# Optimization experiments

Measured on AMD Instinct MI355X. Metric: run time of the kernel, lower is better.

Reference implementation:

```python
import jax, jax.numpy as jnp
import numpy as np

D_MODEL = 1024
N_HEADS = 16
D_HEAD = D_MODEL // N_HEADS
D_FF = 4096
B, T = 2, 2048
EPS = 1e-6


def setup_inputs() -> dict:
    key = jax.random.key(0)
    ks = jax.random.split(key, 10)
    s = 0.02
    return {
        "x": jax.random.normal(ks[0], (B, T, D_MODEL), dtype=jnp.float32),
        # Linear weights stored as (in, out) so y = x @ W (equivalent to torch x @ W.T)
        "Wq": jax.random.normal(ks[1], (D_MODEL, D_MODEL), dtype=jnp.float32) * s,
        "Wk": jax.random.normal(ks[2], (D_MODEL, D_MODEL), dtype=jnp.float32) * s,
        "Wv": jax.random.normal(ks[3], (D_MODEL, D_MODEL), dtype=jnp.float32) * s,
        "Wo": jax.random.normal(ks[4], (D_MODEL, D_MODEL), dtype=jnp.float32) * s,
        "W1": jax.random.normal(ks[5], (D_MODEL, D_FF), dtype=jnp.float32) * s,
        "b1": jnp.zeros((D_FF,), dtype=jnp.float32),
        "W2": jax.random.normal(ks[6], (D_FF, D_MODEL), dtype=jnp.float32) * s,
        "b2": jnp.zeros((D_MODEL,), dtype=jnp.float32),
        "g1": jnp.ones((D_MODEL,), dtype=jnp.float32),
        "g2": jnp.ones((D_MODEL,), dtype=jnp.float32),
    }


def rmsnorm(x, g):
    return x * jax.lax.rsqrt(jnp.mean(x * x, axis=-1, keepdims=True) + EPS) * g


def attention(x, Wq, Wk, Wv, Wo):
    b, t, c = x.shape
    def split_heads(y):  # [B,T,C] -> [B,H,T,Dh]
        return y.reshape(b, t, N_HEADS, D_HEAD).transpose(0, 2, 1, 3)
    q = split_heads(x @ Wq)
    k = split_heads(x @ Wk)
    v = split_heads(x @ Wv)
    att = jnp.einsum("bhqd,bhkd->bhqk", q, k) / jnp.sqrt(jnp.float32(D_HEAD))
    causal = jnp.tril(jnp.ones((t, t), dtype=bool))
    att = jnp.where(causal[None, None], att, -jnp.inf)
    att = jax.nn.softmax(att, axis=-1)
    y = jnp.einsum("bhqk,bhkd->bhqd", att, v)
    y = y.transpose(0, 2, 1, 3).reshape(b, t, c)
    return y @ Wo


def reference(x, Wq, Wk, Wv, Wo, W1, b1, W2, b2, g1, g2):
    x = x + attention(rmsnorm(x, g1), Wq, Wk, Wv, Wo)
    h = rmsnorm(x, g2)
    h = jax.nn.gelu(h @ W1 + b1, approximate=False) @ W2 + b2
    return x + h
```

## Files before the change

### kernel.cpp

```cpp
#include <hip/hip_runtime.h>
#include <hip/hip_bf16.h>
#include <math.h>
#include <stdint.h>


typedef __bf16 v8bf  __attribute__((ext_vector_type(8)));
typedef float  v4f   __attribute__((ext_vector_type(4)));

#define T_SEQ 2048
#define EXP2F(x) __builtin_amdgcn_exp2f(x)

#define FRAG(base, R, ko) \
  (*(const v8bf*)((base) + (R) * 64 + (((((ko) >> 3) ^ ((R) & 7))) << 3)))

__device__ __forceinline__ void async_ld16(const void* g, void* l) {
  __builtin_amdgcn_global_load_lds(
      (const __attribute__((address_space(1))) uint32_t*)g,
      (__attribute__((address_space(3))) uint32_t*)l, 16, 0, 0);
}

__global__ __launch_bounds__(256) void transpose_w(
    const float* __restrict__ W, __hip_bfloat16* __restrict__ WT,
    int K, int N, int ldo)
{
  __shared__ float tile[32][33];
  const int n0 = blockIdx.x * 32, k0 = blockIdx.y * 32;
  const int tx = threadIdx.x, ty = threadIdx.y;
#pragma unroll
  for (int i = 0; i < 32; i += 8)
    tile[ty + i][tx] = W[(size_t)(k0 + ty + i) * N + n0 + tx];
  __syncthreads();
#pragma unroll
  for (int i = 0; i < 32; i += 8)
    WT[(size_t)(n0 + ty + i) * ldo + k0 + tx] = __float2bfloat16(tile[tx][ty + i]);
}

__global__ __launch_bounds__(256) void transpose_v(
    const __hip_bfloat16* __restrict__ QKV, __hip_bfloat16* __restrict__ VTg)
{
  __shared__ float tile[32][33];
  const int t0 = blockIdx.x * 32;
  const int bh = blockIdx.y >> 1;
  const int dt = (blockIdx.y & 1) * 32;
  const int b = bh >> 4, h = bh & 15;
  const int tx = threadIdx.x, ty = threadIdx.y;
#pragma unroll
  for (int i = 0; i < 32; i += 8)
    tile[ty + i][tx] = __bfloat162float(
        QKV[(size_t)(b * T_SEQ + t0 + ty + i) * 3072 + 2048 + h * 64 + dt + tx]);
  __syncthreads();
#pragma unroll
  for (int i = 0; i < 32; i += 8)
    VTg[((size_t)bh * 64 + dt + ty + i) * T_SEQ + t0 + tx] =
        __float2bfloat16(tile[tx][ty + i]);
}

__global__ __launch_bounds__(256) void rmsnorm_kernel(
    const float* __restrict__ x, const float* __restrict__ g,
    __hip_bfloat16* __restrict__ out)
{
  const int row = blockIdx.x;
  const int t = threadIdx.x;
  const float4 v = ((const float4*)(x + (size_t)row * 1024))[t];
  float ss = v.x * v.x + v.y * v.y + v.z * v.z + v.w * v.w;
#pragma unroll
  for (int off = 32; off; off >>= 1) ss += __shfl_xor(ss, off, 64);
  __shared__ float red[4];
  if ((t & 63) == 0) red[t >> 6] = ss;
  __syncthreads();
  ss = red[0] + red[1] + red[2] + red[3];
  const float rs = rsqrtf(ss * (1.0f / 1024.0f) + 1e-6f);
  const float4 gv = ((const float4*)g)[t];
  __hip_bfloat16* o = out + (size_t)row * 1024 + t * 4;
  o[0] = __float2bfloat16(v.x * rs * gv.x);
  o[1] = __float2bfloat16(v.y * rs * gv.y);
  o[2] = __float2bfloat16(v.z * rs * gv.z);
  o[3] = __float2bfloat16(v.w * rs * gv.w);
}

template <int MODE, int MT>
__global__ __launch_bounds__(256, 2) void gemm_bt(
    const __hip_bfloat16* __restrict__ A,
    const __hip_bfloat16* __restrict__ BT,
    const float* __restrict__ bias,
    const float* __restrict__ resid,
    __hip_bfloat16* __restrict__ outb,
    float* __restrict__ outf,
    int M, int N, int K)
{
  __shared__ __align__(16) __hip_bfloat16 As[32 * MT * 64];
  __shared__ __align__(16) __hip_bfloat16 Bs[128 * 64];
  const int tid = threadIdx.x;
  const int wave = tid >> 6, lane = tid & 63;
  const int quad = lane >> 4, l16 = lane & 15;
  const int m0 = blockIdx.y * (32 * MT), n0 = blockIdx.x * 128;
  const int wr = (wave >> 1) * (16 * MT), wc = (wave & 1) * 64;
  const int lrow = lane >> 3;
  const int scol = ((lane & 7) ^ lrow) * 8;

  v4f acc[MT][4];
#pragma unroll
  for (int i = 0; i < MT; i++)
#pragma unroll
    for (int j = 0; j < 4; j++)
#pragma unroll
      for (int c = 0; c < 4; c++) acc[i][j][c] = 0.0f;

  for (int k0 = 0; k0 < K; k0 += 64) {
#pragma unroll
    for (int i = 0; i < MT + 4; i++) {
      const int c = wave * (MT + 4) + i;
      if (c < 4 * MT) {
        async_ld16(A + (size_t)(m0 + c * 8 + lrow) * K + k0 + scol, As + c * 512);
      } else {
        const int cb = c - 4 * MT;
        async_ld16(BT + (size_t)(n0 + cb * 8 + lrow) * K + k0 + scol, Bs + cb * 512);
      }
    }
    __syncthreads();
#pragma unroll
    for (int ks = 0; ks < 64; ks += 32) {
      v8bf af[MT], bf[4];
#pragma unroll
      for (int mt = 0; mt < MT; mt++)
        af[mt] = FRAG(As, wr + mt * 16 + l16, ks + quad * 8);
#pragma unroll
      for (int nt = 0; nt < 4; nt++)
        bf[nt] = FRAG(Bs, wc + nt * 16 + l16, ks + quad * 8);
#pragma unroll
      for (int mt = 0; mt < MT; mt++)
#pragma unroll
        for (int nt = 0; nt < 4; nt++)
          acc[mt][nt] = __builtin_amdgcn_mfma_f32_16x16x32_bf16(
              af[mt], bf[nt], acc[mt][nt], 0, 0, 0);
    }
    __syncthreads();
  }

#pragma unroll
  for (int mt = 0; mt < MT; mt++) {
#pragma unroll
    for (int r = 0; r < 4; r++) {
      const int gm = m0 + wr + mt * 16 + quad * 4 + r;
#pragma unroll
      for (int nt = 0; nt < 4; nt++) {
        const int gn = n0 + wc + nt * 16 + l16;
        float v = acc[mt][nt][r];
        if (MODE == 0) {
          outb[(size_t)gm * N + gn] = __float2bfloat16(v);
        } else if (MODE == 1) {
          outf[(size_t)gm * N + gn] = resid[(size_t)gm * N + gn] + v;
        } else if (MODE == 2) {
          v += bias[gn];
          v = 0.5f * v * (1.0f + erff(v * 0.70710678118654752f));
          outb[(size_t)gm * N + gn] = __float2bfloat16(v);
        } else {
          v += bias[gn];
          outf[(size_t)gm * N + gn] = resid[(size_t)gm * N + gn] + v;
        }
      }
    }
  }
}

__global__ __launch_bounds__(256, 2) void attn_kernel(
    const __hip_bfloat16* __restrict__ QKV,
    const __hip_bfloat16* __restrict__ VTg,
    __hip_bfloat16* __restrict__ Y)
{
  __shared__ __align__(16) __hip_bfloat16 Ks[2 * 64 * 64];
  __shared__ __align__(16) __hip_bfloat16 Vs[2 * 64 * 64];
  __shared__ __align__(16) __hip_bfloat16 PsA[64 * 64];
  __shared__ __align__(16) __hip_bfloat16 PsB[64 * 64];

  const int tid = threadIdx.x;
  const int wave = tid >> 6, lane = tid & 63;
  const int quad = lane >> 4, l16 = lane & 15;
  const int blk = blockIdx.x;
  const int p = blk & 15, h = (blk >> 4) & 15, b = blk >> 8;
  const int qa = p, qb = 31 - p, kmax = qb;
  const size_t rowbase = (size_t)b * T_SEQ;
  const size_t vbase = (size_t)(b * 16 + h) * 64;
  const int lrow = lane >> 3, scol = ((lane & 7) ^ (lane >> 3)) * 8;

  const float QSC = 0.125f * 1.44269504f;
  v8bf aqA[2], aqB[2];
#pragma unroll
  for (int ks = 0; ks < 2; ks++) {
    v8bf q = *(const v8bf*)(QKV + (rowbase + qa * 64 + wave * 16 + l16) * 3072 +
                            h * 64 + ks * 32 + quad * 8);
#pragma unroll
    for (int j = 0; j < 8; j++) aqA[ks][j] = (__bf16)((float)q[j] * QSC);
    q = *(const v8bf*)(QKV + (rowbase + qb * 64 + wave * 16 + l16) * 3072 +
                       h * 64 + ks * 32 + quad * 8);
#pragma unroll
    for (int j = 0; j < 8; j++) aqB[ks][j] = (__bf16)((float)q[j] * QSC);
  }

  v4f oA[4], oB[4];
  float lpA[4], lpB[4];
#pragma unroll
  for (int i = 0; i < 4; i++) {
    lpA[i] = 0.0f; lpB[i] = 0.0f;
#pragma unroll
    for (int c = 0; c < 4; c++) { oA[i][c] = 0.0f; oB[i][c] = 0.0f; }
  }

  auto stage = [&](int kt, int buf) {
#pragma unroll
    for (int i = 0; i < 2; i++) {
      const int r8 = i * 32 + wave * 8;
      const int rr = r8 + lrow;
      async_ld16(QKV + (rowbase + kt * 64 + rr) * 3072 + 1024 + h * 64 + scol,
                 Ks + buf * 4096 + r8 * 64);
      async_ld16(VTg + (vbase + rr) * T_SEQ + kt * 64 + scol,
                 Vs + buf * 4096 + r8 * 64);
    }
  };
  stage(0, 0);

  auto softmax_store = [&](v4f s[4], float lp[4], __hip_bfloat16* Ps, bool diag) {
    if (diag) {
#pragma unroll
      for (int nt = 0; nt < 4; nt++) {
        const int colr = nt * 16 + l16;
#pragma unroll
        for (int r = 0; r < 4; r++)
          if (colr > wave * 16 + quad * 4 + r) s[nt][r] = -30000.0f;
      }
    }
#pragma unroll
    for (int r = 0; r < 4; r++) {
      const int row = wave * 16 + quad * 4 + r;
      const int rsw = (quad * 4 + r) & 7;
#pragma unroll
      for (int nt = 0; nt < 4; nt++) {
        const float e = EXP2F(s[nt][r]);
        lp[r] += e;
        const int chunk = (nt * 2 + (l16 >> 3)) ^ rsw;
        Ps[row * 64 + (chunk << 3) + (l16 & 7)] = __float2bfloat16(e);
      }
    }
  };

  for (int kt = 0; kt <= kmax; kt++) {
    __syncthreads();
    if (kt < kmax) stage(kt + 1, (kt + 1) & 1);
    const __hip_bfloat16* Kb = Ks + (kt & 1) * 4096;
    const __hip_bfloat16* Vb = Vs + (kt & 1) * 4096;
    const bool doA = (kt <= qa);

    {
      v8bf kf[2][4];
#pragma unroll
      for (int ks = 0; ks < 2; ks++)
#pragma unroll
        for (int nt = 0; nt < 4; nt++)
          kf[ks][nt] = FRAG(Kb, nt * 16 + l16, ks * 32 + quad * 8);

      v4f sB[4];
#pragma unroll
      for (int nt = 0; nt < 4; nt++)
#pragma unroll
        for (int c = 0; c < 4; c++) sB[nt][c] = 0.0f;
#pragma unroll
      for (int ks = 0; ks < 2; ks++)
#pragma unroll
        for (int nt = 0; nt < 4; nt++)
          sB[nt] = __builtin_amdgcn_mfma_f32_16x16x32_bf16(aqB[ks], kf[ks][nt],
                                                           sB[nt], 0, 0, 0);
      softmax_store(sB, lpB, PsB, kt == qb);

      if (doA) {
        v4f sA[4];
#pragma unroll
        for (int nt = 0; nt < 4; nt++)
#pragma unroll
          for (int c = 0; c < 4; c++) sA[nt][c] = 0.0f;
#pragma unroll
        for (int ks = 0; ks < 2; ks++)
#pragma unroll
          for (int nt = 0; nt < 4; nt++)
            sA[nt] = __builtin_amdgcn_mfma_f32_16x16x32_bf16(aqA[ks], kf[ks][nt],
                                                             sA[nt], 0, 0, 0);
        softmax_store(sA, lpA, PsA, kt == qa);
      }
    }

    {
      v8bf vf[2][4];
#pragma unroll
      for (int ks = 0; ks < 2; ks++)
#pragma unroll
        for (int nt = 0; nt < 4; nt++)
          vf[ks][nt] = FRAG(Vb, nt * 16 + l16, ks * 32 + quad * 8);
#pragma unroll
      for (int ks = 0; ks < 2; ks++) {
        const v8bf apB = FRAG(PsB, wave * 16 + l16, ks * 32 + quad * 8);
#pragma unroll
        for (int nt = 0; nt < 4; nt++)
          oB[nt] = __builtin_amdgcn_mfma_f32_16x16x32_bf16(apB, vf[ks][nt],
                                                           oB[nt], 0, 0, 0);
      }
      if (doA) {
#pragma unroll
        for (int ks = 0; ks < 2; ks++) {
          const v8bf apA = FRAG(PsA, wave * 16 + l16, ks * 32 + quad * 8);
#pragma unroll
          for (int nt = 0; nt < 4; nt++)
            oA[nt] = __builtin_amdgcn_mfma_f32_16x16x32_bf16(apA, vf[ks][nt],
                                                             oA[nt], 0, 0, 0);
        }
      }
    }
  }

#pragma unroll
  for (int r = 0; r < 4; r++) {
    float la = lpA[r], lb = lpB[r];
#pragma unroll
    for (int off = 1; off < 16; off <<= 1) {
      la += __shfl_xor(la, off, 16);
      lb += __shfl_xor(lb, off, 16);
    }
    const float ila = 1.0f / la, ilb = 1.0f / lb;
#pragma unroll
    for (int nt = 0; nt < 4; nt++) {
      Y[(rowbase + qa * 64 + wave * 16 + quad * 4 + r) * 1024 + h * 64 + nt * 16 + l16] =
          __float2bfloat16(oA[nt][r] * ila);
      Y[(rowbase + qb * 64 + wave * 16 + quad * 4 + r) * 1024 + h * 64 + nt * 16 + l16] =
          __float2bfloat16(oB[nt][r] * ilb);
    }
  }
}

extern "C" void kernel_launch(void* const* d_in, const int* in_sizes, int n_in,
                              void* d_out, int out_size, void* d_ws, size_t ws_size,
                              hipStream_t stream)
{
  const float* x  = (const float*)d_in[0];
  const float* Wq = (const float*)d_in[1];
  const float* Wk = (const float*)d_in[2];
  const float* Wv = (const float*)d_in[3];
  const float* Wo = (const float*)d_in[4];
  const float* W1 = (const float*)d_in[5];
  const float* b1 = (const float*)d_in[6];
  const float* W2 = (const float*)d_in[7];
  const float* b2 = (const float*)d_in[8];
  const float* g1 = (const float*)d_in[9];
  const float* g2 = (const float*)d_in[10];

  uint8_t* ws = (uint8_t*)d_ws;
  __hip_bfloat16* WqkvT = (__hip_bfloat16*)(ws + 0);
  __hip_bfloat16* WoT   = (__hip_bfloat16*)(ws + 6291456);
  __hip_bfloat16* W1T   = (__hip_bfloat16*)(ws + 8388608);
  __hip_bfloat16* W2T   = (__hip_bfloat16*)(ws + 16777216);
  float*          x1    = (float*)(ws + 25165824);
  __hip_bfloat16* VTg   = (__hip_bfloat16*)(ws + 25165824);
  __hip_bfloat16* xn    = (__hip_bfloat16*)(ws + 41943040);
  __hip_bfloat16* QKV   = (__hip_bfloat16*)(ws + 50331648);
  __hip_bfloat16* Ybuf  = (__hip_bfloat16*)(ws + 75497472);
  __hip_bfloat16* Hbuf  = (__hip_bfloat16*)(ws + 50331648);

  const dim3 tb(32, 8);
  transpose_w<<<dim3(32, 32), tb, 0, stream>>>(Wq, WqkvT,               1024, 1024, 1024);
  transpose_w<<<dim3(32, 32), tb, 0, stream>>>(Wk, WqkvT + 1024 * 1024, 1024, 1024, 1024);
  transpose_w<<<dim3(32, 32), tb, 0, stream>>>(Wv, WqkvT + 2048 * 1024, 1024, 1024, 1024);
  transpose_w<<<dim3(32, 32), tb, 0, stream>>>(Wo, WoT, 1024, 1024, 1024);
  transpose_w<<<dim3(128, 32), tb, 0, stream>>>(W1, W1T, 1024, 4096, 1024);
  transpose_w<<<dim3(32, 128), tb, 0, stream>>>(W2, W2T, 4096, 1024, 4096);

  rmsnorm_kernel<<<4096, 256, 0, stream>>>(x, g1, xn);
  gemm_bt<0, 4><<<dim3(24, 32), 256, 0, stream>>>(xn, WqkvT, nullptr, nullptr, QKV,
                                                  nullptr, 4096, 3072, 1024);
  transpose_v<<<dim3(64, 64), tb, 0, stream>>>(QKV, VTg);
  attn_kernel<<<512, 256, 0, stream>>>(QKV, VTg, Ybuf);
  gemm_bt<1, 2><<<dim3(8, 64), 256, 0, stream>>>(Ybuf, WoT, nullptr, x, nullptr, x1,
                                                 4096, 1024, 1024);
  rmsnorm_kernel<<<4096, 256, 0, stream>>>(x1, g2, xn);
  gemm_bt<2, 4><<<dim3(32, 32), 256, 0, stream>>>(xn, W1T, b1, nullptr, Hbuf, nullptr,
                                                  4096, 4096, 1024);
  gemm_bt<3, 2><<<dim3(8, 64), 256, 0, stream>>>(Hbuf, W2T, b2, x1, nullptr,
                                                 (float*)d_out, 4096, 1024, 4096);
}
```

Before: 343.5 us.

## Register-prefetch GEMM tiles, raise occupancy bound, merge four weight transposes

The GEMM drops the async global-to-LDS loads. It now prefetches the next K tile into registers while the current tile's MFMAs run, then stores those registers to swizzled LDS after a barrier, which overlaps global latency with compute. The launch-bounds occupancy hint goes from 2 to 3 or 4 blocks per SM depending on MT, which limits registers per thread and may cause spills given the extra prefetch registers. The four 1024x1024 weight transposes are merged into one launch using a z-grid, relying on WoT sitting right after WqkvT in the workspace.

```diff
diff --git a/kernel.cpp b/kernel.cpp
--- a/kernel.cpp
+++ b/kernel.cpp
@@ -17,6 +17,26 @@
   __builtin_amdgcn_global_load_lds(
       (const __attribute__((address_space(1))) uint32_t*)g,
       (__attribute__((address_space(3))) uint32_t*)l, 16, 0, 0);
+}
+
+__global__ __launch_bounds__(256) void transpose_w4(
+    const float* __restrict__ Wq, const float* __restrict__ Wk,
+    const float* __restrict__ Wv, const float* __restrict__ Wo,
+    __hip_bfloat16* __restrict__ out)
+{
+  __shared__ float tile[32][33];
+  const int z = blockIdx.z;
+  const float* W = z == 0 ? Wq : z == 1 ? Wk : z == 2 ? Wv : Wo;
+  const int n0 = blockIdx.x * 32, k0 = blockIdx.y * 32;
+  const int tx = threadIdx.x, ty = threadIdx.y;
+#pragma unroll
+  for (int i = 0; i < 32; i += 8)
+    tile[ty + i][tx] = W[(size_t)(k0 + ty + i) * 1024 + n0 + tx];
+  __syncthreads();
+  __hip_bfloat16* o = out + (size_t)z * 1024 * 1024;
+#pragma unroll
+  for (int i = 0; i < 32; i += 8)
+    o[(size_t)(n0 + ty + i) * 1024 + k0 + tx] = __float2bfloat16(tile[tx][ty + i]);
 }
 
 __global__ __launch_bounds__(256) void transpose_w(
@@ -79,7 +99,7 @@
 }
 
 template <int MODE, int MT>
-__global__ __launch_bounds__(256, 2) void gemm_bt(
+__global__ __launch_bounds__(256, MT == 4 ? 3 : 4) void gemm_bt(
     const __hip_bfloat16* __restrict__ A,
     const __hip_bfloat16* __restrict__ BT,
     const float* __restrict__ bias,
@@ -96,7 +116,33 @@
   const int m0 = blockIdx.y * (32 * MT), n0 = blockIdx.x * 128;
   const int wr = (wave >> 1) * (16 * MT), wc = (wave & 1) * 64;
   const int lrow = lane >> 3;
-  const int scol = ((lane & 7) ^ lrow) * 8;
+  const int gcol = (lane & 7) * 8;
+  const int swoff = ((lane & 7) ^ lrow) * 8;
+
+  const __hip_bfloat16* agp[MT];
+  const __hip_bfloat16* bgp[4];
+  __hip_bfloat16* alp[MT];
+  __hip_bfloat16* blp[4];
+#pragma unroll
+  for (int i = 0; i < MT; i++) {
+    const int c = wave * MT + i;
+    agp[i] = A + (size_t)(m0 + c * 8 + lrow) * K + gcol;
+    alp[i] = As + c * 512 + lrow * 64 + swoff;
+  }
+#pragma unroll
+  for (int i = 0; i < 4; i++) {
+    const int c = wave * 4 + i;
+    bgp[i] = BT + (size_t)(n0 + c * 8 + lrow) * K + gcol;
+    blp[i] = Bs + c * 512 + lrow * 64 + swoff;
+  }
+
+  uint4 ra[MT], rb[4];
+  auto gload = [&](int k0) {
+#pragma unroll
+    for (int i = 0; i < MT; i++) ra[i] = *(const uint4*)(agp[i] + k0);
+#pragma unroll
+    for (int i = 0; i < 4; i++) rb[i] = *(const uint4*)(bgp[i] + k0);
+  };
 
   v4f acc[MT][4];
 #pragma unroll
@@ -106,18 +152,15 @@
 #pragma unroll
       for (int c = 0; c < 4; c++) acc[i][j][c] = 0.0f;
 
+  gload(0);
   for (int k0 = 0; k0 < K; k0 += 64) {
-#pragma unroll
-    for (int i = 0; i < MT + 4; i++) {
-      const int c = wave * (MT + 4) + i;
-      if (c < 4 * MT) {
-        async_ld16(A + (size_t)(m0 + c * 8 + lrow) * K + k0 + scol, As + c * 512);
-      } else {
-        const int cb = c - 4 * MT;
-        async_ld16(BT + (size_t)(n0 + cb * 8 + lrow) * K + k0 + scol, Bs + cb * 512);
-      }
-    }
     __syncthreads();
+#pragma unroll
+    for (int i = 0; i < MT; i++) *(uint4*)alp[i] = ra[i];
+#pragma unroll
+    for (int i = 0; i < 4; i++) *(uint4*)blp[i] = rb[i];
+    __syncthreads();
+    if (k0 + 64 < K) gload(k0 + 64);
 #pragma unroll
     for (int ks = 0; ks < 64; ks += 32) {
       v8bf af[MT], bf[4];
@@ -134,7 +177,6 @@
           acc[mt][nt] = __builtin_amdgcn_mfma_f32_16x16x32_bf16(
               af[mt], bf[nt], acc[mt][nt], 0, 0, 0);
     }
-    __syncthreads();
   }
 
 #pragma unroll
@@ -363,10 +405,7 @@
   __hip_bfloat16* Hbuf  = (__hip_bfloat16*)(ws + 50331648);
 
   const dim3 tb(32, 8);
-  transpose_w<<<dim3(32, 32), tb, 0, stream>>>(Wq, WqkvT,               1024, 1024, 1024);
-  transpose_w<<<dim3(32, 32), tb, 0, stream>>>(Wk, WqkvT + 1024 * 1024, 1024, 1024, 1024);
-  transpose_w<<<dim3(32, 32), tb, 0, stream>>>(Wv, WqkvT + 2048 * 1024, 1024, 1024, 1024);
-  transpose_w<<<dim3(32, 32), tb, 0, stream>>>(Wo, WoT, 1024, 1024, 1024);
+  transpose_w4<<<dim3(32, 32, 4), tb, 0, stream>>>(Wq, Wk, Wv, Wo, WqkvT);
   transpose_w<<<dim3(128, 32), tb, 0, stream>>>(W1, W1T, 1024, 4096, 1024);
   transpose_w<<<dim3(32, 128), tb, 0, stream>>>(W2, W2T, 4096, 1024, 4096);
 
```

After: 775.2 us. +125.7%, slower.

## Split-K the W2 GEMM with atomic accumulation and merge Q/K/V/O weight transposes

Applied to the files above, without the earlier changes.

The final FFN down-projection GEMM is split along K into two halves (grid z=2), and each half atomically adds its partial result into the output. The output is pre-initialised with residual plus bias inside the second rmsnorm kernel. The four 1024x1024 weight transposes are folded into one launch, and workspace buffers are reassigned so VT and Y no longer alias x1. This doubles the block count for the K=4096 GEMM, which otherwise launches only 512 blocks, and cuts launch count, at the cost of fp32 atomics traffic and non-deterministic summation order.

```diff
diff --git a/kernel.cpp b/kernel.cpp
--- a/kernel.cpp
+++ b/kernel.cpp
@@ -17,6 +17,26 @@
   __builtin_amdgcn_global_load_lds(
       (const __attribute__((address_space(1))) uint32_t*)g,
       (__attribute__((address_space(3))) uint32_t*)l, 16, 0, 0);
+}
+
+__global__ __launch_bounds__(256) void transpose_w4(
+    const float* __restrict__ Wq, const float* __restrict__ Wk,
+    const float* __restrict__ Wv, const float* __restrict__ Wo,
+    __hip_bfloat16* __restrict__ out)
+{
+  __shared__ float tile[32][33];
+  const int z = blockIdx.z;
+  const float* W = z == 0 ? Wq : z == 1 ? Wk : z == 2 ? Wv : Wo;
+  const int n0 = blockIdx.x * 32, k0 = blockIdx.y * 32;
+  const int tx = threadIdx.x, ty = threadIdx.y;
+#pragma unroll
+  for (int i = 0; i < 32; i += 8)
+    tile[ty + i][tx] = W[(size_t)(k0 + ty + i) * 1024 + n0 + tx];
+  __syncthreads();
+  __hip_bfloat16* o = out + (size_t)z * 1024 * 1024;
+#pragma unroll
+  for (int i = 0; i < 32; i += 8)
+    o[(size_t)(n0 + ty + i) * 1024 + k0 + tx] = __float2bfloat16(tile[tx][ty + i]);
 }
 
 __global__ __launch_bounds__(256) void transpose_w(
@@ -57,7 +77,8 @@
 
 __global__ __launch_bounds__(256) void rmsnorm_kernel(
     const float* __restrict__ x, const float* __restrict__ g,
-    __hip_bfloat16* __restrict__ out)
+    __hip_bfloat16* __restrict__ out,
+    const float* __restrict__ bias, float* __restrict__ dinit)
 {
   const int row = blockIdx.x;
   const int t = threadIdx.x;
@@ -76,6 +97,12 @@
   o[1] = __float2bfloat16(v.y * rs * gv.y);
   o[2] = __float2bfloat16(v.z * rs * gv.z);
   o[3] = __float2bfloat16(v.w * rs * gv.w);
+  if (dinit) {
+    const float4 bv = ((const float4*)bias)[t];
+    float4 d;
+    d.x = v.x + bv.x; d.y = v.y + bv.y; d.z = v.z + bv.z; d.w = v.w + bv.w;
+    ((float4*)(dinit + (size_t)row * 1024))[t] = d;
+  }
 }
 
 template <int MODE, int MT>
@@ -86,7 +113,7 @@
     const float* __restrict__ resid,
     __hip_bfloat16* __restrict__ outb,
     float* __restrict__ outf,
-    int M, int N, int K)
+    int M, int N, int K, int Ksub)
 {
   __shared__ __align__(16) __hip_bfloat16 As[32 * MT * 64];
   __shared__ __align__(16) __hip_bfloat16 Bs[128 * 64];
@@ -94,6 +121,7 @@
   const int wave = tid >> 6, lane = tid & 63;
   const int quad = lane >> 4, l16 = lane & 15;
   const int m0 = blockIdx.y * (32 * MT), n0 = blockIdx.x * 128;
+  const size_t kb = (size_t)blockIdx.z * Ksub;
   const int wr = (wave >> 1) * (16 * MT), wc = (wave & 1) * 64;
   const int lrow = lane >> 3;
   const int scol = ((lane & 7) ^ lrow) * 8;
@@ -106,15 +134,16 @@
 #pragma unroll
       for (int c = 0; c < 4; c++) acc[i][j][c] = 0.0f;
 
-  for (int k0 = 0; k0 < K; k0 += 64) {
+  for (int k0 = 0; k0 < Ksub; k0 += 64) {
 #pragma unroll
     for (int i = 0; i < MT + 4; i++) {
       const int c = wave * (MT + 4) + i;
       if (c < 4 * MT) {
-        async_ld16(A + (size_t)(m0 + c * 8 + lrow) * K + k0 + scol, As + c * 512);
+        async_ld16(A + (size_t)(m0 + c * 8 + lrow) * K + kb + k0 + scol, As + c * 512);
       } else {
         const int cb = c - 4 * MT;
-        async_ld16(BT + (size_t)(n0 + cb * 8 + lrow) * K + k0 + scol, Bs + cb * 512);
+        async_ld16(BT + (size_t)(n0 + cb * 8 + lrow) * K + kb + k0 + scol,
+                   Bs + cb * 512);
       }
     }
     __syncthreads();
@@ -155,8 +184,7 @@
           v = 0.5f * v * (1.0f + erff(v * 0.70710678118654752f));
           outb[(size_t)gm * N + gn] = __float2bfloat16(v);
         } else {
-          v += bias[gn];
-          outf[(size_t)gm * N + gn] = resid[(size_t)gm * N + gn] + v;
+          atomicAdd(&outf[(size_t)gm * N + gn], v);
         }
       }
     }
@@ -356,30 +384,28 @@
   __hip_bfloat16* W1T   = (__hip_bfloat16*)(ws + 8388608);
   __hip_bfloat16* W2T   = (__hip_bfloat16*)(ws + 16777216);
   float*          x1    = (float*)(ws + 25165824);
-  __hip_bfloat16* VTg   = (__hip_bfloat16*)(ws + 25165824);
   __hip_bfloat16* xn    = (__hip_bfloat16*)(ws + 41943040);
+  __hip_bfloat16* Ybuf  = (__hip_bfloat16*)(ws + 41943040);
   __hip_bfloat16* QKV   = (__hip_bfloat16*)(ws + 50331648);
-  __hip_bfloat16* Ybuf  = (__hip_bfloat16*)(ws + 75497472);
+  __hip_bfloat16* VTg   = (__hip_bfloat16*)(ws + 75497472);
   __hip_bfloat16* Hbuf  = (__hip_bfloat16*)(ws + 50331648);
 
   const dim3 tb(32, 8);
-  transpose_w<<<dim3(32, 32), tb, 0, stream>>>(Wq, WqkvT,               1024, 1024, 1024);
-  transpose_w<<<dim3(32, 32), tb, 0, stream>>>(Wk, WqkvT + 1024 * 1024, 1024, 1024, 1024);
-  transpose_w<<<dim3(32, 32), tb, 0, stream>>>(Wv, WqkvT + 2048 * 1024, 1024, 1024, 1024);
-  transpose_w<<<dim3(32, 32), tb, 0, stream>>>(Wo, WoT, 1024, 1024, 1024);
+  transpose_w4<<<dim3(32, 32, 4), tb, 0, stream>>>(Wq, Wk, Wv, Wo, WqkvT);
   transpose_w<<<dim3(128, 32), tb, 0, stream>>>(W1, W1T, 1024, 4096, 1024);
   transpose_w<<<dim3(32, 128), tb, 0, stream>>>(W2, W2T, 4096, 1024, 4096);
 
-  rmsnorm_kernel<<<4096, 256, 0, stream>>>(x, g1, xn);
+  rmsnorm_kernel<<<4096, 256, 0, stream>>>(x, g1, xn, nullptr, nullptr);
   gemm_bt<0, 4><<<dim3(24, 32), 256, 0, stream>>>(xn, WqkvT, nullptr, nullptr, QKV,
-                                                  nullptr, 4096, 3072, 1024);
+                                                  nullptr, 4096, 3072, 1024, 1024);
   transpose_v<<<dim3(64, 64), tb, 0, stream>>>(QKV, VTg);
   attn_kernel<<<512, 256, 0, stream>>>(QKV, VTg, Ybuf);
   gemm_bt<1, 2><<<dim3(8, 64), 256, 0, stream>>>(Ybuf, WoT, nullptr, x, nullptr, x1,
-                                                 4096, 1024, 1024);
-  rmsnorm_kernel<<<4096, 256, 0, stream>>>(x1, g2, xn);
+                                                 4096, 1024, 1024, 1024);
+  rmsnorm_kernel<<<4096, 256, 0, stream>>>(x1, g2, xn, b2, (float*)d_out);
   gemm_bt<2, 4><<<dim3(32, 32), 256, 0, stream>>>(xn, W1T, b1, nullptr, Hbuf, nullptr,
-                                                  4096, 4096, 1024);
-  gemm_bt<3, 2><<<dim3(8, 64), 256, 0, stream>>>(Hbuf, W2T, b2, x1, nullptr,
-                                                 (float*)d_out, 4096, 1024, 4096);
-}
+                                                  4096, 4096, 1024, 1024);
+  gemm_bt<4, 2><<<dim3(8, 64, 2), 256, 0, stream>>>(Hbuf, W2T, nullptr, nullptr,
+                                                    nullptr, (float*)d_out,
+                                                    4096, 1024, 4096, 2048);
+}
```

After: 346.4 us. Within noise of the previous version (+0.8%).
